# Performance work log

Hardware: AMD Instinct MI355X
Metric: run time of the kernel (lower is better)

Reference implementation:

```python
import jax, jax.numpy as jnp
import numpy as np

B = 100        # number of queries
N = 50000      # n_node
E = 600000     # n_edges
D = 128        # in_dim = out_dim (hidden_dim)
A = 64         # attn_dim
R = 200        # n_rel -> rela_embed has 2*R+1 = 401 rows


def setup_inputs() -> dict:
    key = jax.random.key(0)
    ks = jax.random.split(key, 14)
    q_sub = jax.random.randint(ks[0], (B,), 0, N)
    q_rel = jax.random.randint(ks[1], (B,), 0, 2 * R + 1)
    # edges: [E, 6]; col0=r_idx(<B), col2=rel(<2R+1), col4=sub(<N), col5=obj(<N); cols 1,3 unused
    c0 = jax.random.randint(ks[2], (E,), 0, B)
    c2 = jax.random.randint(ks[3], (E,), 0, 2 * R + 1)
    c4 = jax.random.randint(ks[4], (E,), 0, N)
    c5 = jax.random.randint(ks[5], (E,), 0, N)
    z = jnp.zeros((E,), dtype=jnp.int32)
    edges = jnp.stack([c0, z, c2, z, c4, c5], axis=1)
    hidden = jax.random.normal(ks[6], (N, D), dtype=jnp.float32)
    # learned parameters
    rela_embed = jax.random.normal(ks[7], (2 * R + 1, D), dtype=jnp.float32) * 0.02
    Ws = jax.random.normal(ks[8], (D, A), dtype=jnp.float32) * 0.05   # Ws_attn.weight^T
    Wr = jax.random.normal(ks[9], (D, A), dtype=jnp.float32) * 0.05   # Wr_attn.weight^T
    Wqr = jax.random.normal(ks[10], (D, A), dtype=jnp.float32) * 0.05 # Wqr_attn.weight^T
    bqr = jnp.zeros((A,), dtype=jnp.float32)
    wa = jax.random.normal(ks[11], (A, 1), dtype=jnp.float32) * 0.05  # w_alpha.weight^T
    ba = jnp.zeros((1,), dtype=jnp.float32)
    Wh = jax.random.normal(ks[12], (D, D), dtype=jnp.float32) * 0.05  # W_h.weight^T
    return {"q_sub": q_sub, "q_rel": q_rel, "hidden": hidden, "edges": edges,
            "n_node": N, "rela_embed": rela_embed, "Ws": Ws, "Wr": Wr,
            "Wqr": Wqr, "bqr": bqr, "wa": wa, "ba": ba, "Wh": Wh}


def reference(q_sub, q_rel, hidden, edges, n_node, rela_embed, Ws, Wr, Wqr, bqr, wa, ba, Wh):
    sub = edges[:, 4]
    rel = edges[:, 2]
    obj = edges[:, 5]
    r_idx = edges[:, 0]
    hs = hidden[sub]                       # [E, D] gather
    hr = rela_embed[rel]                   # [E, D] gather
    h_qr = rela_embed[q_rel][r_idx]        # [B, D] then gather -> [E, D]
    # attention score per edge
    pre = hs @ Ws + hr @ Wr + h_qr @ Wqr + bqr          # [E, A]
    alpha = jax.nn.sigmoid(jax.nn.relu(pre) @ wa + ba)   # [E, 1]
    message = alpha * (hs + hr)                          # [E, D]
    message_agg = jax.ops.segment_sum(message, obj, num_segments=n_node)  # [N, D]
    hidden_new = message_agg @ Wh                        # act = identity ('idd')
    return hidden_new
```

## Files before the change

### kernel.cpp

```cpp
#include <hip/hip_runtime.h>

#define DD 128
#define AA 64
#define SS 96

static inline int idiv_up(int a, int b) { return (a + b - 1) / b; }

__device__ __forceinline__ unsigned short f2bf(float f) {
    unsigned u = __float_as_uint(f);
    u += 0x7fff + ((u >> 16) & 1);
    return (unsigned short)(u >> 16);
}
__device__ __forceinline__ float bf2f(unsigned short h) {
    return __uint_as_float(((unsigned)h) << 16);
}

__global__ __launch_bounds__(256)
void proj_all_kernel(const float* __restrict__ hidden,
                     const float* __restrict__ rela,
                     const int* __restrict__ q_rel,
                     const float* __restrict__ Ws,
                     const float* __restrict__ Wr,
                     const float* __restrict__ Wqr,
                     const float* __restrict__ bqr,
                     const float* __restrict__ Wh,
                     float* __restrict__ subrows,
                     float* __restrict__ hrWr,
                     float* __restrict__ relaWh,
                     float* __restrict__ hqrWqr,
                     int N, int NR, int B, int nA, int nB) {
    __shared__ float lht[128 * 64];
    const int t = threadIdx.x;
    const int bid = blockIdx.x;
    int type, rbase, nrows;
    const float* src;
    if (bid < nA)           { type = 0; rbase = bid * 64;             nrows = N;  src = hidden; }
    else if (bid < nA + nB) { type = 1; rbase = (bid - nA) * 64;      nrows = NR; src = rela; }
    else                    { type = 2; rbase = (bid - nA - nB) * 64; nrows = B;  src = rela; }

    const int row = t & 63;
    const int d0 = (t >> 6) * 32;
    const int gr = rbase + row;
    const float* srow = nullptr;
    if (gr < nrows) {
        const int sr = (type == 2) ? q_rel[gr] : gr;
        srow = src + (long)sr * DD;
    }
    #pragma unroll
    for (int j = 0; j < 8; ++j) {
        float4 v = make_float4(0.f, 0.f, 0.f, 0.f);
        if (srow) v = *(const float4*)&srow[d0 + j * 4];
        lht[(d0 + j * 4 + 0) * 64 + row] = v.x;
        lht[(d0 + j * 4 + 1) * 64 + row] = v.y;
        lht[(d0 + j * 4 + 2) * 64 + row] = v.z;
        lht[(d0 + j * 4 + 3) * 64 + row] = v.w;
    }
    __syncthreads();

    const int r0 = (t & 15) * 4;
    const int c0 = (t >> 4) * 4;
    const int nph = (type == 2) ? 1 : 3;

    for (int p = 0; p < nph; ++p) {
        const float* W;
        int ldw, off;
        if (p == 0) {
            W = (type == 0) ? Ws : (type == 1) ? Wr : Wqr;
            ldw = 64; off = 0;
        } else {
            W = Wh; ldw = 128; off = (p - 1) * 64;
        }
        const float* wp = W + off + c0;

        float acc[4][4] = {};
        #pragma unroll 4
        for (int d = 0; d < 128; ++d) {
            const float4 hv = *(const float4*)&lht[d * 64 + r0];
            const float4 wv = *(const float4*)&wp[(long)d * ldw];
            acc[0][0] = fmaf(hv.x, wv.x, acc[0][0]);
            acc[0][1] = fmaf(hv.x, wv.y, acc[0][1]);
            acc[0][2] = fmaf(hv.x, wv.z, acc[0][2]);
            acc[0][3] = fmaf(hv.x, wv.w, acc[0][3]);
            acc[1][0] = fmaf(hv.y, wv.x, acc[1][0]);
            acc[1][1] = fmaf(hv.y, wv.y, acc[1][1]);
            acc[1][2] = fmaf(hv.y, wv.z, acc[1][2]);
            acc[1][3] = fmaf(hv.y, wv.w, acc[1][3]);
            acc[2][0] = fmaf(hv.z, wv.x, acc[2][0]);
            acc[2][1] = fmaf(hv.z, wv.y, acc[2][1]);
            acc[2][2] = fmaf(hv.z, wv.z, acc[2][2]);
            acc[2][3] = fmaf(hv.z, wv.w, acc[2][3]);
            acc[3][0] = fmaf(hv.w, wv.x, acc[3][0]);
            acc[3][1] = fmaf(hv.w, wv.y, acc[3][1]);
            acc[3][2] = fmaf(hv.w, wv.z, acc[3][2]);
            acc[3][3] = fmaf(hv.w, wv.w, acc[3][3]);
        }

        #pragma unroll
        for (int i = 0; i < 4; ++i) {
            const int orow = rbase + r0 + i;
            if (orow >= nrows) continue;
            if (type == 0) {
                float* srw = subrows + (long)orow * SS;
                ushort4 o;
                o.x = f2bf(acc[i][0]); o.y = f2bf(acc[i][1]);
                o.z = f2bf(acc[i][2]); o.w = f2bf(acc[i][3]);
                if (p == 0) {
                    *(ushort4*)((unsigned short*)srw + c0) = o;
                } else {
                    *(ushort4*)((unsigned short*)(srw + 32) + off + c0) = o;
                }
            } else if (type == 1) {
                if (p == 0) {
                    *(float4*)&hrWr[(long)orow * 64 + c0] =
                        make_float4(acc[i][0], acc[i][1], acc[i][2], acc[i][3]);
                } else {
                    *(float4*)&relaWh[(long)orow * 128 + off + c0] =
                        make_float4(acc[i][0], acc[i][1], acc[i][2], acc[i][3]);
                }
            } else {
                const float4 bq = *(const float4*)&bqr[c0];
                *(float4*)&hqrWqr[(long)orow * 64 + c0] =
                    make_float4(acc[i][0] + bq.x, acc[i][1] + bq.y,
                                acc[i][2] + bq.z, acc[i][3] + bq.w);
            }
        }
    }
}

__global__ void hist_kernel(const int* __restrict__ edges, int* deg, int E) {
    const int e = blockIdx.x * blockDim.x + threadIdx.x;
    if (e < E) atomicAdd(&deg[edges[(long)e * 6 + 5]], 1);
}

__global__ __launch_bounds__(256)
void scan_kernel(const int* __restrict__ deg, int* __restrict__ loff,
                 int* __restrict__ cur, int* __restrict__ bsum,
                 int* __restrict__ bsumx, int* __restrict__ done,
                 int n, int nb) {
    __shared__ int tsum[256];
    __shared__ int lastFlag;
    const int t = threadIdx.x;
    const int b = blockIdx.x;
    const int base = b * 1024 + t * 4;
    int v[4];
    int s = 0;
    #pragma unroll
    for (int j = 0; j < 4; ++j) {
        v[j] = (base + j < n) ? deg[base + j] : 0;
        s += v[j];
    }
    tsum[t] = s;
    __syncthreads();
    for (int o = 1; o < 256; o <<= 1) {
        const int x = (t >= o) ? tsum[t - o] : 0;
        __syncthreads();
        tsum[t] += x;
        __syncthreads();
    }
    int run = (t > 0) ? tsum[t - 1] : 0;
    #pragma unroll
    for (int j = 0; j < 4; ++j) {
        if (base + j < n) { loff[base + j] = run; cur[base + j] = run; }
        run += v[j];
    }
    if (t == 255) {
        bsum[b] = tsum[255];
        __threadfence();
    }
    __syncthreads();
    if (t == 0) lastFlag = (atomicAdd(done, 1) == nb - 1);
    __syncthreads();
    if (lastFlag && t < 64) {
        __threadfence();
        const int val = (t < nb) ? bsum[t] : 0;
        int inc = val;
        #pragma unroll
        for (int o = 1; o < 64; o <<= 1) {
            const int x = __shfl_up(inc, o, 64);
            if (t >= o) inc += x;
        }
        if (t < nb) bsumx[t] = inc - val;
    }
}

__global__ void scatter_kernel(const int* __restrict__ edges, int* cur,
                               const int* __restrict__ bsumx,
                               int2* __restrict__ recs, int E) {
    const int e = blockIdx.x * blockDim.x + threadIdx.x;
    if (e >= E) return;
    const int2 a = *(const int2*)&edges[(long)e * 6];
    const int2 b = *(const int2*)&edges[(long)e * 6 + 2];
    const int2 c = *(const int2*)&edges[(long)e * 6 + 4];
    const int pos = bsumx[c.y >> 10] + atomicAdd(&cur[c.y], 1);
    recs[pos] = make_int2(c.x, b.x | (a.x << 16));
}

__global__ __launch_bounds__(256)
void gather_kernel(const int2* __restrict__ recs,
                   const int* __restrict__ loff,
                   const int* __restrict__ bsumx,
                   const float* __restrict__ subrows,
                   const float* __restrict__ hrWr,
                   const float* __restrict__ hqrWqr,
                   const float* __restrict__ relaWh,
                   const float* __restrict__ wa,
                   const float* __restrict__ ba,
                   float* __restrict__ out, int N, int E) {
    const int lane = threadIdx.x & 63;
    const int g = lane >> 4;
    const int l = lane & 15;
    const int v = (int)((blockIdx.x * blockDim.x + threadIdx.x) >> 6);
    if (v >= N) return;
    const float4 wav = *(const float4*)&wa[l * 4];
    const float bar = ba[0];
    const int start = loff[v] + bsumx[v >> 10];
    const int end = (v + 1 < N) ? (loff[v + 1] + bsumx[(v + 1) >> 10]) : E;

    float4 acc0 = make_float4(0.f, 0.f, 0.f, 0.f);
    float4 acc1 = make_float4(0.f, 0.f, 0.f, 0.f);

    for (int base = start; base < end; base += 8) {
        const int k1 = base + g;
        const int k2 = base + 4 + g;
        const bool va1 = (k1 < end);
        const bool va2 = (k2 < end);
        const int2 rc1 = va1 ? recs[k1] : make_int2(0, 0);
        const int2 rc2 = va2 ? recs[k2] : make_int2(0, 0);
        const int sub1 = rc1.x, rel1 = rc1.y & 0xffff, rid1 = rc1.y >> 16;
        const int sub2 = rc2.x, rel2 = rc2.y & 0xffff, rid2 = rc2.y >> 16;
        const float* sr1 = subrows + (long)sub1 * SS;
        const float* sr2 = subrows + (long)sub2 * SS;

        const ushort4 hw1 = *(const ushort4*)((const unsigned short*)sr1 + l * 4);
        const ushort4 hw2 = *(const ushort4*)((const unsigned short*)sr2 + l * 4);
        const float4 b41 = *(const float4*)&hrWr[rel1 * AA + l * 4];
        const float4 b42 = *(const float4*)&hrWr[rel2 * AA + l * 4];
        const float4 c41 = *(const float4*)&hqrWqr[rid1 * AA + l * 4];
        const float4 c42 = *(const float4*)&hqrWqr[rid2 * AA + l * 4];
        const ushort4 m01 = *(const ushort4*)((const unsigned short*)(sr1 + 32) + l * 8);
        const ushort4 m11 = *(const ushort4*)((const unsigned short*)(sr1 + 32) + l * 8 + 4);
        const ushort4 m02 = *(const ushort4*)((const unsigned short*)(sr2 + 32) + l * 8);
        const ushort4 m12 = *(const ushort4*)((const unsigned short*)(sr2 + 32) + l * 8 + 4);
        const float4 r01 = *(const float4*)&relaWh[rel1 * DD + l * 8];
        const float4 r11 = *(const float4*)&relaWh[rel1 * DD + l * 8 + 4];
        const float4 r02 = *(const float4*)&relaWh[rel2 * DD + l * 8];
        const float4 r12 = *(const float4*)&relaWh[rel2 * DD + l * 8 + 4];

        float s1 = fmaxf(bf2f(hw1.x) + b41.x + c41.x, 0.f) * wav.x;
        s1 = fmaf(fmaxf(bf2f(hw1.y) + b41.y + c41.y, 0.f), wav.y, s1);
        s1 = fmaf(fmaxf(bf2f(hw1.z) + b41.z + c41.z, 0.f), wav.z, s1);
        s1 = fmaf(fmaxf(bf2f(hw1.w) + b41.w + c41.w, 0.f), wav.w, s1);
        float s2 = fmaxf(bf2f(hw2.x) + b42.x + c42.x, 0.f) * wav.x;
        s2 = fmaf(fmaxf(bf2f(hw2.y) + b42.y + c42.y, 0.f), wav.y, s2);
        s2 = fmaf(fmaxf(bf2f(hw2.z) + b42.z + c42.z, 0.f), wav.z, s2);
        s2 = fmaf(fmaxf(bf2f(hw2.w) + b42.w + c42.w, 0.f), wav.w, s2);
        s1 += __shfl_xor(s1, 1);  s2 += __shfl_xor(s2, 1);
        s1 += __shfl_xor(s1, 2);  s2 += __shfl_xor(s2, 2);
        s1 += __shfl_xor(s1, 4);  s2 += __shfl_xor(s2, 4);
        s1 += __shfl_xor(s1, 8);  s2 += __shfl_xor(s2, 8);
        float al1 = __builtin_amdgcn_rcpf(1.0f + __expf(-(s1 + bar)));
        float al2 = __builtin_amdgcn_rcpf(1.0f + __expf(-(s2 + bar)));
        if (!va1) al1 = 0.0f;
        if (!va2) al2 = 0.0f;

        acc0.x = fmaf(al1, bf2f(m01.x) + r01.x, acc0.x);
        acc0.y = fmaf(al1, bf2f(m01.y) + r01.y, acc0.y);
        acc0.z = fmaf(al1, bf2f(m01.z) + r01.z, acc0.z);
        acc0.w = fmaf(al1, bf2f(m01.w) + r01.w, acc0.w);
        acc1.x = fmaf(al1, bf2f(m11.x) + r11.x, acc1.x);
        acc1.y = fmaf(al1, bf2f(m11.y) + r11.y, acc1.y);
        acc1.z = fmaf(al1, bf2f(m11.z) + r11.z, acc1.z);
        acc1.w = fmaf(al1, bf2f(m11.w) + r11.w, acc1.w);
        acc0.x = fmaf(al2, bf2f(m02.x) + r02.x, acc0.x);
        acc0.y = fmaf(al2, bf2f(m02.y) + r02.y, acc0.y);
        acc0.z = fmaf(al2, bf2f(m02.z) + r02.z, acc0.z);
        acc0.w = fmaf(al2, bf2f(m02.w) + r02.w, acc0.w);
        acc1.x = fmaf(al2, bf2f(m12.x) + r12.x, acc1.x);
        acc1.y = fmaf(al2, bf2f(m12.y) + r12.y, acc1.y);
        acc1.z = fmaf(al2, bf2f(m12.z) + r12.z, acc1.z);
        acc1.w = fmaf(al2, bf2f(m12.w) + r12.w, acc1.w);
    }

    #pragma unroll
    for (int o = 16; o <= 32; o <<= 1) {
        acc0.x += __shfl_xor(acc0.x, o);
        acc0.y += __shfl_xor(acc0.y, o);
        acc0.z += __shfl_xor(acc0.z, o);
        acc0.w += __shfl_xor(acc0.w, o);
        acc1.x += __shfl_xor(acc1.x, o);
        acc1.y += __shfl_xor(acc1.y, o);
        acc1.z += __shfl_xor(acc1.z, o);
        acc1.w += __shfl_xor(acc1.w, o);
    }
    if (g == 0) {
        *(float4*)&out[(long)v * DD + l * 8]     = acc0;
        *(float4*)&out[(long)v * DD + l * 8 + 4] = acc1;
    }
}

extern "C" void kernel_launch(void* const* d_in, const int* in_sizes, int n_in,
                              void* d_out, int out_size, void* d_ws, size_t ws_size,
                              hipStream_t stream) {
    const int*   q_rel  = (const int*)d_in[1];
    const float* hidden = (const float*)d_in[2];
    const int*   edges  = (const int*)d_in[3];
    const float* rela   = (const float*)d_in[5];
    const float* Ws     = (const float*)d_in[6];
    const float* Wr     = (const float*)d_in[7];
    const float* Wqr    = (const float*)d_in[8];
    const float* bqr    = (const float*)d_in[9];
    const float* wa     = (const float*)d_in[10];
    const float* ba     = (const float*)d_in[11];
    const float* Wh     = (const float*)d_in[12];

    const int B  = in_sizes[1];
    const int N  = in_sizes[2] / DD;
    const int E  = in_sizes[3] / 6;
    const int NR = in_sizes[5] / DD;

    float* out = (float*)d_out;

    float* subrows = (float*)d_ws;
    float* hrWr    = subrows + (size_t)N * SS;
    float* relaWh  = hrWr + (size_t)NR * AA;
    float* hqrWqr  = relaWh + (size_t)NR * DD;
    int*   deg     = (int*)(hqrWqr + (size_t)B * AA);
    int*   done    = deg + N;
    int*   cur     = done + 3;
    int*   loff    = cur + N;
    int*   bsum    = loff + N;
    int*   bsumx   = bsum + 64;
    int2*  recs    = (int2*)(bsumx + 64);

    const int nA = idiv_up(N, 64);
    const int nB = idiv_up(NR, 64);
    const int nC = idiv_up(B, 64);
    const int nb = idiv_up(N, 1024);

    hipMemsetAsync(deg, 0, (size_t)(N + 1) * sizeof(int), stream);
    proj_all_kernel<<<nA + nB + nC, 256, 0, stream>>>(
        hidden, rela, q_rel, Ws, Wr, Wqr, bqr, Wh,
        subrows, hrWr, relaWh, hqrWqr, N, NR, B, nA, nB);
    hist_kernel<<<idiv_up(E, 256), 256, 0, stream>>>(edges, deg, E);
    scan_kernel<<<nb, 256, 0, stream>>>(deg, loff, cur, bsum, bsumx, done, N, nb);
    scatter_kernel<<<idiv_up(E, 256), 256, 0, stream>>>(edges, cur, bsumx, recs, E);
    gather_kernel<<<idiv_up(N * 64, 256), 256, 0, stream>>>(
        recs, loff, bsumx, subrows, hrWr, hqrWqr, relaWh, wa, ba, out, N, E);
}
```

Before: 289.5 us.

## Fuse projection phases into one pass and vectorize edge loads in hist/scatter

The projection kernel now computes the attention weight product and both halves of the Wh product in a single loop over d, using 48 accumulators instead of three separate passes. Each staged LDS value is read once rather than three times, at the cost of higher register pressure. The histogram and scatter kernels now process four edges per thread with int4 loads of the packed 6-int edge rows, which cuts load instructions and launches a quarter of the threads. The per-thread work in those kernels becomes serial, which reduces parallelism for hiding atomic latency.

```diff
diff --git a/kernel.cpp b/kernel.cpp
--- a/kernel.cpp
+++ b/kernel.cpp
@@ -59,77 +59,81 @@
 
     const int r0 = (t & 15) * 4;
     const int c0 = (t >> 4) * 4;
-    const int nph = (type == 2) ? 1 : 3;
-
-    for (int p = 0; p < nph; ++p) {
-        const float* W;
-        int ldw, off;
-        if (p == 0) {
-            W = (type == 0) ? Ws : (type == 1) ? Wr : Wqr;
-            ldw = 64; off = 0;
-        } else {
-            W = Wh; ldw = 128; off = (p - 1) * 64;
-        }
-        const float* wp = W + off + c0;
-
-        float acc[4][4] = {};
-        #pragma unroll 4
-        for (int d = 0; d < 128; ++d) {
-            const float4 hv = *(const float4*)&lht[d * 64 + r0];
-            const float4 wv = *(const float4*)&wp[(long)d * ldw];
-            acc[0][0] = fmaf(hv.x, wv.x, acc[0][0]);
-            acc[0][1] = fmaf(hv.x, wv.y, acc[0][1]);
-            acc[0][2] = fmaf(hv.x, wv.z, acc[0][2]);
-            acc[0][3] = fmaf(hv.x, wv.w, acc[0][3]);
-            acc[1][0] = fmaf(hv.y, wv.x, acc[1][0]);
-            acc[1][1] = fmaf(hv.y, wv.y, acc[1][1]);
-            acc[1][2] = fmaf(hv.y, wv.z, acc[1][2]);
-            acc[1][3] = fmaf(hv.y, wv.w, acc[1][3]);
-            acc[2][0] = fmaf(hv.z, wv.x, acc[2][0]);
-            acc[2][1] = fmaf(hv.z, wv.y, acc[2][1]);
-            acc[2][2] = fmaf(hv.z, wv.z, acc[2][2]);
-            acc[2][3] = fmaf(hv.z, wv.w, acc[2][3]);
-            acc[3][0] = fmaf(hv.w, wv.x, acc[3][0]);
-            acc[3][1] = fmaf(hv.w, wv.y, acc[3][1]);
-            acc[3][2] = fmaf(hv.w, wv.z, acc[3][2]);
-            acc[3][3] = fmaf(hv.w, wv.w, acc[3][3]);
-        }
-
+
+    const float* W0 = ((type == 0) ? Ws : (type == 1) ? Wr : Wqr) + c0;
+    const float* W1 = Wh + c0;
+    const float* W2 = Wh + 64 + c0;
+
+    float acc[4][12] = {};
+    #pragma unroll 4
+    for (int d = 0; d < 128; ++d) {
+        const float4 hv  = *(const float4*)&lht[d * 64 + r0];
+        const float4 wv0 = *(const float4*)&W0[(long)d * 64];
+        const float4 wv1 = *(const float4*)&W1[(long)d * 128];
+        const float4 wv2 = *(const float4*)&W2[(long)d * 128];
+        const float h[4] = { hv.x, hv.y, hv.z, hv.w };
         #pragma unroll
         for (int i = 0; i < 4; ++i) {
-            const int orow = rbase + r0 + i;
-            if (orow >= nrows) continue;
-            if (type == 0) {
-                float* srw = subrows + (long)orow * SS;
-                ushort4 o;
-                o.x = f2bf(acc[i][0]); o.y = f2bf(acc[i][1]);
-                o.z = f2bf(acc[i][2]); o.w = f2bf(acc[i][3]);
-                if (p == 0) {
-                    *(ushort4*)((unsigned short*)srw + c0) = o;
-                } else {
-                    *(ushort4*)((unsigned short*)(srw + 32) + off + c0) = o;
-                }
-            } else if (type == 1) {
-                if (p == 0) {
-                    *(float4*)&hrWr[(long)orow * 64 + c0] =
-                        make_float4(acc[i][0], acc[i][1], acc[i][2], acc[i][3]);
-                } else {
-                    *(float4*)&relaWh[(long)orow * 128 + off + c0] =
-                        make_float4(acc[i][0], acc[i][1], acc[i][2], acc[i][3]);
-                }
-            } else {
-                const float4 bq = *(const float4*)&bqr[c0];
-                *(float4*)&hqrWqr[(long)orow * 64 + c0] =
-                    make_float4(acc[i][0] + bq.x, acc[i][1] + bq.y,
-                                acc[i][2] + bq.z, acc[i][3] + bq.w);
-            }
+            acc[i][0]  = fmaf(h[i], wv0.x, acc[i][0]);
+            acc[i][1]  = fmaf(h[i], wv0.y, acc[i][1]);
+            acc[i][2]  = fmaf(h[i], wv0.z, acc[i][2]);
+            acc[i][3]  = fmaf(h[i], wv0.w, acc[i][3]);
+            acc[i][4]  = fmaf(h[i], wv1.x, acc[i][4]);
+            acc[i][5]  = fmaf(h[i], wv1.y, acc[i][5]);
+            acc[i][6]  = fmaf(h[i], wv1.z, acc[i][6]);
+            acc[i][7]  = fmaf(h[i], wv1.w, acc[i][7]);
+            acc[i][8]  = fmaf(h[i], wv2.x, acc[i][8]);
+            acc[i][9]  = fmaf(h[i], wv2.y, acc[i][9]);
+            acc[i][10] = fmaf(h[i], wv2.z, acc[i][10]);
+            acc[i][11] = fmaf(h[i], wv2.w, acc[i][11]);
+        }
+    }
+
+    #pragma unroll
+    for (int i = 0; i < 4; ++i) {
+        const int orow = rbase + r0 + i;
+        if (orow >= nrows) continue;
+        if (type == 0) {
+            float* srw = subrows + (long)orow * SS;
+            ushort4 o0, o1, o2;
+            o0.x = f2bf(acc[i][0]);  o0.y = f2bf(acc[i][1]);
+            o0.z = f2bf(acc[i][2]);  o0.w = f2bf(acc[i][3]);
+            o1.x = f2bf(acc[i][4]);  o1.y = f2bf(acc[i][5]);
+            o1.z = f2bf(acc[i][6]);  o1.w = f2bf(acc[i][7]);
+            o2.x = f2bf(acc[i][8]);  o2.y = f2bf(acc[i][9]);
+            o2.z = f2bf(acc[i][10]); o2.w = f2bf(acc[i][11]);
+            *(ushort4*)((unsigned short*)srw + c0) = o0;
+            *(ushort4*)((unsigned short*)(srw + 32) + c0) = o1;
+            *(ushort4*)((unsigned short*)(srw + 32) + 64 + c0) = o2;
+        } else if (type == 1) {
+            *(float4*)&hrWr[(long)orow * 64 + c0] =
+                make_float4(acc[i][0], acc[i][1], acc[i][2], acc[i][3]);
+            *(float4*)&relaWh[(long)orow * 128 + c0] =
+                make_float4(acc[i][4], acc[i][5], acc[i][6], acc[i][7]);
+            *(float4*)&relaWh[(long)orow * 128 + 64 + c0] =
+                make_float4(acc[i][8], acc[i][9], acc[i][10], acc[i][11]);
+        } else {
+            const float4 bq = *(const float4*)&bqr[c0];
+            *(float4*)&hqrWqr[(long)orow * 64 + c0] =
+                make_float4(acc[i][0] + bq.x, acc[i][1] + bq.y,
+                            acc[i][2] + bq.z, acc[i][3] + bq.w);
         }
     }
 }
 
 __global__ void hist_kernel(const int* __restrict__ edges, int* deg, int E) {
-    const int e = blockIdx.x * blockDim.x + threadIdx.x;
-    if (e < E) atomicAdd(&deg[edges[(long)e * 6 + 5]], 1);
+    const int e0 = (blockIdx.x * blockDim.x + threadIdx.x) * 4;
+    if (e0 >= E) return;
+    if (e0 + 3 < E) {
+        const int4* p = (const int4*)&edges[(long)e0 * 6];
+        const int4 j1 = p[1], j2 = p[2], j4 = p[4], j5 = p[5];
+        atomicAdd(&deg[j1.y], 1);
+        atomicAdd(&deg[j2.w], 1);
+        atomicAdd(&deg[j4.y], 1);
+        atomicAdd(&deg[j5.w], 1);
+    } else {
+        for (int e = e0; e < E; ++e) atomicAdd(&deg[edges[(long)e * 6 + 5]], 1);
+    }
 }
 
 __global__ __launch_bounds__(256)
@@ -186,13 +190,35 @@
 __global__ void scatter_kernel(const int* __restrict__ edges, int* cur,
                                const int* __restrict__ bsumx,
                                int2* __restrict__ recs, int E) {
-    const int e = blockIdx.x * blockDim.x + threadIdx.x;
-    if (e >= E) return;
-    const int2 a = *(const int2*)&edges[(long)e * 6];
-    const int2 b = *(const int2*)&edges[(long)e * 6 + 2];
-    const int2 c = *(const int2*)&edges[(long)e * 6 + 4];
-    const int pos = bsumx[c.y >> 10] + atomicAdd(&cur[c.y], 1);
-    recs[pos] = make_int2(c.x, b.x | (a.x << 16));
+    const int e0 = (blockIdx.x * blockDim.x + threadIdx.x) * 4;
+    if (e0 >= E) return;
+    if (e0 + 3 < E) {
+        const int4* p = (const int4*)&edges[(long)e0 * 6];
+        const int4 j0 = p[0], j1 = p[1], j2 = p[2], j3 = p[3], j4 = p[4], j5 = p[5];
+        {
+            const int pos = bsumx[j1.y >> 10] + atomicAdd(&cur[j1.y], 1);
+            recs[pos] = make_int2(j1.x, j0.z | (j0.x << 16));
+        }
+        {
+            const int pos = bsumx[j2.w >> 10] + atomicAdd(&cur[j2.w], 1);
+            recs[pos] = make_int2(j2.z, j2.x | (j1.z << 16));
+        }
+        {
+            const int pos = bsumx[j4.y >> 10] + atomicAdd(&cur[j4.y], 1);
+            recs[pos] = make_int2(j4.x, j3.z | (j3.x << 16));
+        }
+        {
+            const int pos = bsumx[j5.w >> 10] + atomicAdd(&cur[j5.w], 1);
+            recs[pos] = make_int2(j5.z, j5.x | (j4.z << 16));
+        }
+    } else {
+        for (int e = e0; e < E; ++e) {
+            const int* ed = edges + (long)e * 6;
+            const int obj = ed[5];
+            const int pos = bsumx[obj >> 10] + atomicAdd(&cur[obj], 1);
+            recs[pos] = make_int2(ed[4], ed[2] | (ed[0] << 16));
+        }
+    }
 }
 
 __global__ __launch_bounds__(256)
@@ -341,9 +367,9 @@
     proj_all_kernel<<<nA + nB + nC, 256, 0, stream>>>(
         hidden, rela, q_rel, Ws, Wr, Wqr, bqr, Wh,
         subrows, hrWr, relaWh, hqrWqr, N, NR, B, nA, nB);
-    hist_kernel<<<idiv_up(E, 256), 256, 0, stream>>>(edges, deg, E);
+    hist_kernel<<<idiv_up(E, 1024), 256, 0, stream>>>(edges, deg, E);
     scan_kernel<<<nb, 256, 0, stream>>>(deg, loff, cur, bsum, bsumx, done, N, nb);
-    scatter_kernel<<<idiv_up(E, 256), 256, 0, stream>>>(edges, cur, bsumx, recs, E);
+    scatter_kernel<<<idiv_up(E, 1024), 256, 0, stream>>>(edges, cur, bsumx, recs, E);
     gather_kernel<<<idiv_up(N * 64, 256), 256, 0, stream>>>(
         recs, loff, bsumx, subrows, hrWr, hqrWqr, relaWh, wa, ba, out, N, E);
 }
```

Result: no change. 290.4 us (+0.3%).
